# Optimization experiments

Hardware: AMD Instinct MI355X
Metric: run time of the kernel (lower is better)

## Reference

```python
import jax, jax.numpy as jnp
import numpy as np

CH = 64
INTER = 8  # max(64 // 8, 1)


def setup_inputs() -> dict:
    key = jax.random.key(0)
    ks = jax.random.split(key, 8)
    B, C, H, W = 4, CH, 64, 64
    x = jax.random.normal(ks[0], (B, C, H, W), dtype=jnp.float32)
    s = 1.0 / np.sqrt(C)
    Wq = jax.random.normal(ks[1], (INTER, C), dtype=jnp.float32) * s
    bq = jnp.zeros((INTER,), dtype=jnp.float32)
    Wk = jax.random.normal(ks[2], (INTER, C), dtype=jnp.float32) * s
    bk = jnp.zeros((INTER,), dtype=jnp.float32)
    Wv = jax.random.normal(ks[3], (C, C), dtype=jnp.float32) * s
    bv = jnp.zeros((C,), dtype=jnp.float32)
    gamma = jax.random.normal(ks[4], (1,), dtype=jnp.float32) * 0.1
    return {"x": x, "Wq": Wq, "bq": bq, "Wk": Wk, "bk": bk, "Wv": Wv, "bv": bv, "gamma": gamma}


def reference(x, Wq, bq, Wk, bk, Wv, bv, gamma):
    B, C, H, W = x.shape
    xf = x.reshape(B, C, H * W)  # [B, C, N]
    # 1x1 convs == per-pixel linear projections
    q = jnp.einsum('dc,bcn->bdn', Wq, xf) + bq[None, :, None]  # [B, d, N]
    k = jnp.einsum('dc,bcn->bdn', Wk, xf) + bk[None, :, None]  # [B, d, N]
    v = jnp.einsum('ec,bcn->ben', Wv, xf) + bv[None, :, None]  # [B, C, N]
    scale = 1.0 / np.sqrt(INTER).astype(np.float32)
    scores = jnp.einsum('bdi,bdj->bij', q, k) * scale  # [B, N, N]
    attn = jax.nn.softmax(scores, axis=-1)
    out = jnp.einsum('bcj,bij->bci', v, attn)  # value @ attn^T
    out = out.reshape(B, C, H, W)
    return gamma[0] * out + x
```

## Files before the change

### kernel.cpp

```cpp
#include <hip/hip_runtime.h>
#include <hip/hip_bf16.h>
#include <stdint.h>

#define BATCH 4
#define CCH   64
#define NPIX  4096
#define DQK   8
#define PXB   128

typedef __attribute__((ext_vector_type(8)))  short bf16x8;
typedef __attribute__((ext_vector_type(16))) float f32x16;
typedef __attribute__((ext_vector_type(4)))  uint32_t u32x4;

static __device__ __forceinline__ short f2bf(float f) {
    union { __hip_bfloat16 h; short s; } u;
    u.h = __float2bfloat16(f);
    return u.s;
}
static __device__ __forceinline__ uint32_t cvt_pk_bf16(float lo, float hi) {
    uint32_t r;
    asm("v_cvt_pk_bf16_f32 %0, %1, %2" : "=v"(r) : "v"(lo), "v"(hi));
    return r;
}

__global__ __launch_bounds__(256) void proj_kernel(
    const float* __restrict__ x,
    const float* __restrict__ Wq, const float* __restrict__ bq,
    const float* __restrict__ Wk, const float* __restrict__ bk,
    const float* __restrict__ Wv, const float* __restrict__ bv,
    short* __restrict__ qo, short* __restrict__ ko, short* __restrict__ vo)
{
    __shared__ float xs[CCH][PXB];
    __shared__ float wv_s[CCH][68];
    __shared__ float wq_s[CCH][DQK];
    __shared__ float wk_s[CCH][DQK];

    const int b  = blockIdx.x >> 5;
    const int n0 = (blockIdx.x & 31) * PXB;
    const int tid = threadIdx.x;

    for (int i = tid; i < CCH*CCH; i += 256) wv_s[i & 63][i >> 6] = Wv[i];
    for (int i = tid; i < CCH*DQK; i += 256) { wq_s[i & 63][i >> 6] = Wq[i]; wk_s[i & 63][i >> 6] = Wk[i]; }
    for (int i = tid; i < CCH*PXB; i += 256) {
        int c = i >> 7, p = i & 127;
        xs[c][p] = x[((size_t)b*CCH + c)*NPIX + n0 + p];
    }
    __syncthreads();

    const int p0 = tid & 31;
    const int g  = tid >> 5;
    const int e0 = g * 8;

    float av[4][8];
    float aq[4], ak[4];
    #pragma unroll
    for (int pi = 0; pi < 4; ++pi) {
        #pragma unroll
        for (int i = 0; i < 8; ++i) av[pi][i] = bv[e0 + i];
        aq[pi] = bq[g]; ak[pi] = bk[g];
    }

    for (int c = 0; c < CCH; ++c) {
        float4 w0 = *(const float4*)&wv_s[c][e0];
        float4 w1 = *(const float4*)&wv_s[c][e0 + 4];
        float wq = wq_s[c][g], wk = wk_s[c][g];
        #pragma unroll
        for (int pi = 0; pi < 4; ++pi) {
            float xv = xs[c][p0 + 32*pi];
            av[pi][0] += w0.x*xv; av[pi][1] += w0.y*xv;
            av[pi][2] += w0.z*xv; av[pi][3] += w0.w*xv;
            av[pi][4] += w1.x*xv; av[pi][5] += w1.y*xv;
            av[pi][6] += w1.z*xv; av[pi][7] += w1.w*xv;
            aq[pi] += wq*xv; ak[pi] += wk*xv;
        }
    }

    const float qscale = 0.51010407112635f;
    const size_t vb = (size_t)b * CCH * NPIX;
    #pragma unroll
    for (int pi = 0; pi < 4; ++pi) {
        const int px = n0 + p0 + 32*pi;
        #pragma unroll
        for (int i = 0; i < 8; ++i)
            vo[vb + (size_t)(e0 + i)*NPIX + px] = f2bf(av[pi][i]);
        const size_t qb = ((size_t)b*NPIX + px)*16 + g;
        qo[qb]     = f2bf(aq[pi] * qscale);
        qo[qb + 8] = 0;
        ko[qb]     = f2bf(ak[pi]);
        ko[qb + 8] = 0;
    }
}

__global__ __launch_bounds__(512, 2) void attn_kernel(
    const short* __restrict__ qg, const short* __restrict__ kg,
    const short* __restrict__ vg,
    const float* __restrict__ x, const float* __restrict__ gamma,
    float* __restrict__ outp)
{
    __shared__ float l_s[8][32];
    __shared__ float linv_s[32];
    __shared__ float acc_all[8][CCH][32];

    const int b  = blockIdx.x >> 7;
    const int i0 = (blockIdx.x & 127) << 5;
    const int tid  = threadIdx.x;
    const int wave = tid >> 6, lane = tid & 63;
    const int hi = lane >> 5, li = lane & 31;

    f32x16 z16;
    #pragma unroll
    for (int r = 0; r < 16; ++r) z16[r] = 0.f;

    const bf16x8 qf = *(const bf16x8*)&qg[((size_t)b*NPIX + i0 + li)*16 + hi*8];

    f32x16 acc0 = z16, acc1 = z16;
    float l_run = 0.f;

    const short* kp = kg + (size_t)b * NPIX * 16;
    const size_t vbase = (size_t)b * CCH * NPIX;
    const short* vrow0 = &vg[vbase + (size_t)li*NPIX];
    const short* vrow1 = vrow0 + (size_t)32*NPIX;

    const int jbeg = wave << 9;

    bf16x8 kc  = *(const bf16x8*)&kp[(size_t)(jbeg + li)*16 + hi*8];
    bf16x8 v00 = *(const bf16x8*)(vrow0 + jbeg + hi*8);
    bf16x8 v01 = *(const bf16x8*)(vrow0 + jbeg + 16 + hi*8);
    bf16x8 v10 = *(const bf16x8*)(vrow1 + jbeg + hi*8);
    bf16x8 v11 = *(const bf16x8*)(vrow1 + jbeg + 16 + hi*8);

    #pragma unroll 2
    for (int t = 0; t < 16; ++t) {
        const int j1 = jbeg + ((t + 1) & 15)*32;
        bf16x8 kn  = *(const bf16x8*)&kp[(size_t)(j1 + li)*16 + hi*8];
        bf16x8 n00 = *(const bf16x8*)(vrow0 + j1 + hi*8);
        bf16x8 n01 = *(const bf16x8*)(vrow0 + j1 + 16 + hi*8);
        bf16x8 n10 = *(const bf16x8*)(vrow1 + j1 + hi*8);
        bf16x8 n11 = *(const bf16x8*)(vrow1 + j1 + 16 + hi*8);

        f32x16 S = __builtin_amdgcn_mfma_f32_32x32x16_bf16(kc, qf, z16, 0, 0, 0);

        #pragma unroll
        for (int r = 0; r < 16; ++r) S[r] = __builtin_amdgcn_exp2f(S[r]);

        {
            float s0 = (S[0]+S[1]) + (S[2]+S[3]);
            float s1 = (S[4]+S[5]) + (S[6]+S[7]);
            float s2 = (S[8]+S[9]) + (S[10]+S[11]);
            float s3 = (S[12]+S[13]) + (S[14]+S[15]);
            l_run += (s0+s1) + (s2+s3);
        }

        uint32_t a01 = cvt_pk_bf16(S[0], S[1]);
        uint32_t a23 = cvt_pk_bf16(S[2], S[3]);
        uint32_t a45 = cvt_pk_bf16(S[4], S[5]);
        uint32_t a67 = cvt_pk_bf16(S[6], S[7]);
        uint32_t a89 = cvt_pk_bf16(S[8], S[9]);
        uint32_t aab = cvt_pk_bf16(S[10], S[11]);
        uint32_t acd = cvt_pk_bf16(S[12], S[13]);
        uint32_t aef = cvt_pk_bf16(S[14], S[15]);
        asm("v_permlane32_swap_b32 %0, %1" : "+v"(a01), "+v"(a45));
        asm("v_permlane32_swap_b32 %0, %1" : "+v"(a23), "+v"(a67));
        asm("v_permlane32_swap_b32 %0, %1" : "+v"(a89), "+v"(acd));
        asm("v_permlane32_swap_b32 %0, %1" : "+v"(aab), "+v"(aef));
        u32x4 pw0 = { a01, a23, a45, a67 };
        u32x4 pw1 = { a89, aab, acd, aef };
        bf16x8 b0 = __builtin_bit_cast(bf16x8, pw0);
        bf16x8 b1 = __builtin_bit_cast(bf16x8, pw1);

        __builtin_amdgcn_s_setprio(1);
        acc0 = __builtin_amdgcn_mfma_f32_32x32x16_bf16(v00, b0, acc0, 0, 0, 0);
        acc1 = __builtin_amdgcn_mfma_f32_32x32x16_bf16(v10, b0, acc1, 0, 0, 0);
        acc0 = __builtin_amdgcn_mfma_f32_32x32x16_bf16(v01, b1, acc0, 0, 0, 0);
        acc1 = __builtin_amdgcn_mfma_f32_32x32x16_bf16(v11, b1, acc1, 0, 0, 0);
        __builtin_amdgcn_s_setprio(0);

        kc = kn; v00 = n00; v01 = n01; v10 = n10; v11 = n11;
    }

    l_run += __shfl_xor(l_run, 32);
    if (hi == 0) l_s[wave][li] = l_run;
    #pragma unroll
    for (int r = 0; r < 16; ++r) {
        int row = (r & 3) + ((r >> 2) << 3) + (hi << 2);
        acc_all[wave][row][li]      = acc0[r];
        acc_all[wave][row + 32][li] = acc1[r];
    }
    __syncthreads();
    if (wave == 0 && hi == 0) {
        float L = 0.f;
        #pragma unroll
        for (int w = 0; w < 8; ++w) L += l_s[w][li];
        linv_s[li] = __builtin_amdgcn_rcpf(L);
    }
    __syncthreads();

    const float g0 = gamma[0];
    for (int idx = tid; idx < CCH*32; idx += 512) {
        int c = idx >> 5, i = idx & 31;
        float s = 0.f;
        #pragma unroll
        for (int w = 0; w < 8; ++w) s += acc_all[w][c][i];
        size_t gidx = vbase + (size_t)c*NPIX + i0 + i;
        outp[gidx] = g0 * (s * linv_s[i]) + x[gidx];
    }
}

extern "C" void kernel_launch(void* const* d_in, const int* in_sizes, int n_in,
                              void* d_out, int out_size, void* d_ws, size_t ws_size,
                              hipStream_t stream) {
    const float* x     = (const float*)d_in[0];
    const float* Wq    = (const float*)d_in[1];
    const float* bq    = (const float*)d_in[2];
    const float* Wk    = (const float*)d_in[3];
    const float* bk    = (const float*)d_in[4];
    const float* Wv    = (const float*)d_in[5];
    const float* bv    = (const float*)d_in[6];
    const float* gamma = (const float*)d_in[7];

    short* qo = (short*)d_ws;
    short* ko = qo + (size_t)BATCH*NPIX*16;
    short* vo = ko + (size_t)BATCH*NPIX*16;

    proj_kernel<<<BATCH*(NPIX/PXB), 256, 0, stream>>>(x, Wq, bq, Wk, bk, Wv, bv, qo, ko, vo);
    attn_kernel<<<BATCH*(NPIX/32), 512, 0, stream>>>(qo, ko, vo, x, gamma, (float*)d_out);
}
```

Baseline: 116.3 us.

## Split attention key range across blocks with separate merge kernel

Splits the key dimension of the attention into four chunks handled by separate 256-thread blocks, each writing partial unnormalized outputs and row sums to workspace. A new merge kernel sums the partials, normalizes, and applies the gamma residual. The software prefetch of K/V for the next iteration is also removed, so loads are issued inside the loop. This raises grid size and occupancy at the cost of an extra launch and about 16 MB of partial-buffer global traffic.

```diff
diff --git a/kernel.cpp b/kernel.cpp
--- a/kernel.cpp
+++ b/kernel.cpp
@@ -91,18 +91,18 @@
     }
 }
 
-__global__ __launch_bounds__(512, 2) void attn_kernel(
+__global__ __launch_bounds__(256, 4) void attn_main(
     const short* __restrict__ qg, const short* __restrict__ kg,
     const short* __restrict__ vg,
-    const float* __restrict__ x, const float* __restrict__ gamma,
-    float* __restrict__ outp)
+    float* __restrict__ part, float* __restrict__ lp)
 {
-    __shared__ float l_s[8][32];
-    __shared__ float linv_s[32];
-    __shared__ float acc_all[8][CCH][32];
-
-    const int b  = blockIdx.x >> 7;
-    const int i0 = (blockIdx.x & 127) << 5;
+    __shared__ float l_s[4][32];
+    __shared__ float acc_s[4][CCH][32];
+
+    const int jc = blockIdx.x & 3;
+    const int qt = (blockIdx.x >> 2) & 127;
+    const int b  = blockIdx.x >> 9;
+    const int i0 = qt << 5;
     const int tid  = threadIdx.x;
     const int wave = tid >> 6, lane = tid & 63;
     const int hi = lane >> 5, li = lane & 31;
@@ -121,24 +121,18 @@
     const short* vrow0 = &vg[vbase + (size_t)li*NPIX];
     const short* vrow1 = vrow0 + (size_t)32*NPIX;
 
-    const int jbeg = wave << 9;
-
-    bf16x8 kc  = *(const bf16x8*)&kp[(size_t)(jbeg + li)*16 + hi*8];
-    bf16x8 v00 = *(const bf16x8*)(vrow0 + jbeg + hi*8);
-    bf16x8 v01 = *(const bf16x8*)(vrow0 + jbeg + 16 + hi*8);
-    bf16x8 v10 = *(const bf16x8*)(vrow1 + jbeg + hi*8);
-    bf16x8 v11 = *(const bf16x8*)(vrow1 + jbeg + 16 + hi*8);
-
+    const int jbeg = (jc << 10) + (wave << 8);
     #pragma unroll 2
-    for (int t = 0; t < 16; ++t) {
-        const int j1 = jbeg + ((t + 1) & 15)*32;
-        bf16x8 kn  = *(const bf16x8*)&kp[(size_t)(j1 + li)*16 + hi*8];
-        bf16x8 n00 = *(const bf16x8*)(vrow0 + j1 + hi*8);
-        bf16x8 n01 = *(const bf16x8*)(vrow0 + j1 + 16 + hi*8);
-        bf16x8 n10 = *(const bf16x8*)(vrow1 + j1 + hi*8);
-        bf16x8 n11 = *(const bf16x8*)(vrow1 + j1 + 16 + hi*8);
-
-        f32x16 S = __builtin_amdgcn_mfma_f32_32x32x16_bf16(kc, qf, z16, 0, 0, 0);
+    for (int t = 0; t < 8; ++t) {
+        const int j0 = jbeg + t*32;
+
+        bf16x8 akf = *(const bf16x8*)&kp[(size_t)(j0 + li)*16 + hi*8];
+        f32x16 S = __builtin_amdgcn_mfma_f32_32x32x16_bf16(akf, qf, z16, 0, 0, 0);
+
+        bf16x8 av00 = *(const bf16x8*)(vrow0 + j0 + hi*8);
+        bf16x8 av01 = *(const bf16x8*)(vrow0 + j0 + 16 + hi*8);
+        bf16x8 av10 = *(const bf16x8*)(vrow1 + j0 + hi*8);
+        bf16x8 av11 = *(const bf16x8*)(vrow1 + j0 + 16 + hi*8);
 
         #pragma unroll
         for (int r = 0; r < 16; ++r) S[r] = __builtin_amdgcn_exp2f(S[r]);
@@ -169,13 +163,11 @@
         bf16x8 b1 = __builtin_bit_cast(bf16x8, pw1);
 
         __builtin_amdgcn_s_setprio(1);
-        acc0 = __builtin_amdgcn_mfma_f32_32x32x16_bf16(v00, b0, acc0, 0, 0, 0);
-        acc1 = __builtin_amdgcn_mfma_f32_32x32x16_bf16(v10, b0, acc1, 0, 0, 0);
-        acc0 = __builtin_amdgcn_mfma_f32_32x32x16_bf16(v01, b1, acc0, 0, 0, 0);
-        acc1 = __builtin_amdgcn_mfma_f32_32x32x16_bf16(v11, b1, acc1, 0, 0, 0);
+        acc0 = __builtin_amdgcn_mfma_f32_32x32x16_bf16(av00, b0, acc0, 0, 0, 0);
+        acc1 = __builtin_amdgcn_mfma_f32_32x32x16_bf16(av10, b0, acc1, 0, 0, 0);
+        acc0 = __builtin_amdgcn_mfma_f32_32x32x16_bf16(av01, b1, acc0, 0, 0, 0);
+        acc1 = __builtin_amdgcn_mfma_f32_32x32x16_bf16(av11, b1, acc1, 0, 0, 0);
         __builtin_amdgcn_s_setprio(0);
-
-        kc = kn; v00 = n00; v01 = n01; v10 = n10; v11 = n11;
     }
 
     l_run += __shfl_xor(l_run, 32);
@@ -183,24 +175,49 @@
     #pragma unroll
     for (int r = 0; r < 16; ++r) {
         int row = (r & 3) + ((r >> 2) << 3) + (hi << 2);
-        acc_all[wave][row][li]      = acc0[r];
-        acc_all[wave][row + 32][li] = acc1[r];
+        acc_s[wave][row][li]      = acc0[r];
+        acc_s[wave][row + 32][li] = acc1[r];
     }
     __syncthreads();
-    if (wave == 0 && hi == 0) {
-        float L = 0.f;
-        #pragma unroll
-        for (int w = 0; w < 8; ++w) L += l_s[w][li];
-        linv_s[li] = __builtin_amdgcn_rcpf(L);
+
+    float* pb = part + ((size_t)blockIdx.x) * (CCH*32);
+    for (int idx = tid; idx < CCH*32; idx += 256) {
+        int c = idx >> 5, i = idx & 31;
+        pb[idx] = acc_s[0][c][i] + acc_s[1][c][i] + acc_s[2][c][i] + acc_s[3][c][i];
+    }
+    if (tid < 32)
+        lp[((size_t)blockIdx.x)*32 + tid] =
+            l_s[0][tid] + l_s[1][tid] + l_s[2][tid] + l_s[3][tid];
+}
+
+__global__ __launch_bounds__(256) void merge_kernel(
+    const float* __restrict__ part, const float* __restrict__ lp,
+    const float* __restrict__ x, const float* __restrict__ gamma,
+    float* __restrict__ outp)
+{
+    __shared__ float linv_s[32];
+
+    const int qt = blockIdx.x & 127;
+    const int b  = blockIdx.x >> 7;
+    const int tid = threadIdx.x;
+
+    const size_t base = ((size_t)blockIdx.x) * 4 * (CCH*32);
+    const size_t lbase = ((size_t)blockIdx.x) * 4 * 32;
+
+    if (tid < 32) {
+        float L = lp[lbase + tid] + lp[lbase + 32 + tid]
+                + lp[lbase + 64 + tid] + lp[lbase + 96 + tid];
+        linv_s[tid] = __builtin_amdgcn_rcpf(L);
     }
     __syncthreads();
 
     const float g0 = gamma[0];
-    for (int idx = tid; idx < CCH*32; idx += 512) {
+    const size_t vbase = (size_t)b * CCH * NPIX;
+    const int i0 = qt << 5;
+    for (int idx = tid; idx < CCH*32; idx += 256) {
         int c = idx >> 5, i = idx & 31;
-        float s = 0.f;
-        #pragma unroll
-        for (int w = 0; w < 8; ++w) s += acc_all[w][c][i];
+        float s = part[base + idx] + part[base + 2048 + idx]
+                + part[base + 4096 + idx] + part[base + 6144 + idx];
         size_t gidx = vbase + (size_t)c*NPIX + i0 + i;
         outp[gidx] = g0 * (s * linv_s[i]) + x[gidx];
     }
@@ -221,7 +238,10 @@
     short* qo = (short*)d_ws;
     short* ko = qo + (size_t)BATCH*NPIX*16;
     short* vo = ko + (size_t)BATCH*NPIX*16;
+    float* part = (float*)(vo + (size_t)BATCH*CCH*NPIX);
+    float* lp   = part + (size_t)2048*CCH*32;
 
     proj_kernel<<<BATCH*(NPIX/PXB), 256, 0, stream>>>(x, Wq, bq, Wk, bk, Wv, bv, qo, ko, vo);
-    attn_kernel<<<BATCH*(NPIX/32), 512, 0, stream>>>(qo, ko, vo, x, gamma, (float*)d_out);
-}
+    attn_main<<<BATCH*(NPIX/32)*4, 256, 0, stream>>>(qo, ko, vo, part, lp);
+    merge_kernel<<<BATCH*(NPIX/32), 256, 0, stream>>>(part, lp, x, gamma, (float*)d_out);
+}
```

Result: slower. 124.4 us (+7.0%).

## Stage V tiles in swizzled LDS per window and shrink reduction buffer

Applied to the files above, without the earlier changes.

The attention kernel now loads each 256-column V window cooperatively into XOR-swizzled LDS, register-prefetching the next window, and has all waves read their V fragments from shared memory instead of each wave streaming its own disjoint 512-column slice from global memory. The cross-wave reduction reuses a 32KB buffer with a two-phase add, which cuts shared memory and allows a higher occupancy target in launch_bounds (512,4). The cost is two block-wide barriers per window and LDS traffic in the inner loop. The tighter register budget may also cause spills.

```diff
diff --git a/kernel.cpp b/kernel.cpp
--- a/kernel.cpp
+++ b/kernel.cpp
@@ -91,18 +91,22 @@
     }
 }
 
-__global__ __launch_bounds__(512, 2) void attn_kernel(
+__global__ __launch_bounds__(512, 4) void attn_kernel(
     const short* __restrict__ qg, const short* __restrict__ kg,
     const short* __restrict__ vg,
     const float* __restrict__ x, const float* __restrict__ gamma,
     float* __restrict__ outp)
 {
+    __shared__ __align__(16) char smem[32768];
     __shared__ float l_s[8][32];
     __shared__ float linv_s[32];
-    __shared__ float acc_all[8][CCH][32];
-
+
+    char*  vs_c = smem;
+    float* mbuf = (float*)smem;
+
+    const int qt = blockIdx.x & 127;
     const int b  = blockIdx.x >> 7;
-    const int i0 = (blockIdx.x & 127) << 5;
+    const int i0 = qt << 5;
     const int tid  = threadIdx.x;
     const int wave = tid >> 6, lane = tid & 63;
     const int hi = lane >> 5, li = lane & 31;
@@ -118,27 +122,48 @@
 
     const short* kp = kg + (size_t)b * NPIX * 16;
     const size_t vbase = (size_t)b * CCH * NPIX;
-    const short* vrow0 = &vg[vbase + (size_t)li*NPIX];
-    const short* vrow1 = vrow0 + (size_t)32*NPIX;
-
-    const int jbeg = wave << 9;
-
-    bf16x8 kc  = *(const bf16x8*)&kp[(size_t)(jbeg + li)*16 + hi*8];
-    bf16x8 v00 = *(const bf16x8*)(vrow0 + jbeg + hi*8);
-    bf16x8 v01 = *(const bf16x8*)(vrow0 + jbeg + 16 + hi*8);
-    bf16x8 v10 = *(const bf16x8*)(vrow1 + jbeg + hi*8);
-    bf16x8 v11 = *(const bf16x8*)(vrow1 + jbeg + 16 + hi*8);
-
-    #pragma unroll 2
-    for (int t = 0; t < 16; ++t) {
-        const int j1 = jbeg + ((t + 1) & 15)*32;
-        bf16x8 kn  = *(const bf16x8*)&kp[(size_t)(j1 + li)*16 + hi*8];
-        bf16x8 n00 = *(const bf16x8*)(vrow0 + j1 + hi*8);
-        bf16x8 n01 = *(const bf16x8*)(vrow0 + j1 + 16 + hi*8);
-        bf16x8 n10 = *(const bf16x8*)(vrow1 + j1 + hi*8);
-        bf16x8 n11 = *(const bf16x8*)(vrow1 + j1 + 16 + hi*8);
-
-        f32x16 S = __builtin_amdgcn_mfma_f32_32x32x16_bf16(kc, qf, z16, 0, 0, 0);
+
+    const int sc  = tid >> 3;
+    const short* vsrc = vg + vbase + (size_t)sc*NPIX + (tid & 7)*8;
+    const int   wb  = (tid & 7) * 16;
+    const int   swz = (sc & 15) << 4;
+    char* wp = vs_c + sc*512;
+
+    const int  rswz = (li & 15) << 4;
+    const int  rb0  = (wave << 6) + (hi << 4);
+    char* rp0 = vs_c + li*512;
+    char* rp1 = vs_c + (li + 32)*512;
+
+    int4 st0 = *(const int4*)(vsrc);
+    int4 st1 = *(const int4*)(vsrc + 64);
+    int4 st2 = *(const int4*)(vsrc + 128);
+    int4 st3 = *(const int4*)(vsrc + 192);
+    bf16x8 akf = *(const bf16x8*)&kp[(size_t)((wave << 5) + li)*16 + hi*8];
+
+    for (int win = 0; win < 16; ++win) {
+        *(int4*)(wp + ((wb +   0) ^ swz)) = st0;
+        *(int4*)(wp + ((wb + 128) ^ swz)) = st1;
+        *(int4*)(wp + ((wb + 256) ^ swz)) = st2;
+        *(int4*)(wp + ((wb + 384) ^ swz)) = st3;
+        if (win < 15) {
+            const short* ns = vsrc + (win + 1)*256;
+            st0 = *(const int4*)(ns);
+            st1 = *(const int4*)(ns + 64);
+            st2 = *(const int4*)(ns + 128);
+            st3 = *(const int4*)(ns + 192);
+        }
+        __syncthreads();
+
+        f32x16 S = __builtin_amdgcn_mfma_f32_32x32x16_bf16(akf, qf, z16, 0, 0, 0);
+        if (win < 15) {
+            const int jn = ((win + 1) << 8) + (wave << 5);
+            akf = *(const bf16x8*)&kp[(size_t)(jn + li)*16 + hi*8];
+        }
+
+        bf16x8 av00 = *(const bf16x8*)(rp0 + ((rb0     ) ^ rswz));
+        bf16x8 av01 = *(const bf16x8*)(rp0 + ((rb0 + 32) ^ rswz));
+        bf16x8 av10 = *(const bf16x8*)(rp1 + ((rb0     ) ^ rswz));
+        bf16x8 av11 = *(const bf16x8*)(rp1 + ((rb0 + 32) ^ rswz));
 
         #pragma unroll
         for (int r = 0; r < 16; ++r) S[r] = __builtin_amdgcn_exp2f(S[r]);
@@ -169,38 +194,46 @@
         bf16x8 b1 = __builtin_bit_cast(bf16x8, pw1);
 
         __builtin_amdgcn_s_setprio(1);
-        acc0 = __builtin_amdgcn_mfma_f32_32x32x16_bf16(v00, b0, acc0, 0, 0, 0);
-        acc1 = __builtin_amdgcn_mfma_f32_32x32x16_bf16(v10, b0, acc1, 0, 0, 0);
-        acc0 = __builtin_amdgcn_mfma_f32_32x32x16_bf16(v01, b1, acc0, 0, 0, 0);
-        acc1 = __builtin_amdgcn_mfma_f32_32x32x16_bf16(v11, b1, acc1, 0, 0, 0);
+        acc0 = __builtin_amdgcn_mfma_f32_32x32x16_bf16(av00, b0, acc0, 0, 0, 0);
+        acc1 = __builtin_amdgcn_mfma_f32_32x32x16_bf16(av10, b0, acc1, 0, 0, 0);
+        acc0 = __builtin_amdgcn_mfma_f32_32x32x16_bf16(av01, b1, acc0, 0, 0, 0);
+        acc1 = __builtin_amdgcn_mfma_f32_32x32x16_bf16(av11, b1, acc1, 0, 0, 0);
         __builtin_amdgcn_s_setprio(0);
-
-        kc = kn; v00 = n00; v01 = n01; v10 = n10; v11 = n11;
+        __syncthreads();
     }
 
     l_run += __shfl_xor(l_run, 32);
     if (hi == 0) l_s[wave][li] = l_run;
-    #pragma unroll
-    for (int r = 0; r < 16; ++r) {
-        int row = (r & 3) + ((r >> 2) << 3) + (hi << 2);
-        acc_all[wave][row][li]      = acc0[r];
-        acc_all[wave][row + 32][li] = acc1[r];
+
+    if (wave < 4) {
+        #pragma unroll
+        for (int r = 0; r < 16; ++r) {
+            int row = (r & 3) + ((r >> 2) << 3) + (hi << 2);
+            mbuf[(wave*64 + row)*32 + li]      = acc0[r];
+            mbuf[(wave*64 + row + 32)*32 + li] = acc1[r];
+        }
     }
     __syncthreads();
-    if (wave == 0 && hi == 0) {
+    if (wave >= 4) {
+        #pragma unroll
+        for (int r = 0; r < 16; ++r) {
+            int row = (r & 3) + ((r >> 2) << 3) + (hi << 2);
+            mbuf[((wave-4)*64 + row)*32 + li]      += acc0[r];
+            mbuf[((wave-4)*64 + row + 32)*32 + li] += acc1[r];
+        }
+    } else if (tid < 32) {
         float L = 0.f;
         #pragma unroll
-        for (int w = 0; w < 8; ++w) L += l_s[w][li];
-        linv_s[li] = __builtin_amdgcn_rcpf(L);
+        for (int w = 0; w < 8; ++w) L += l_s[w][tid];
+        linv_s[tid] = __builtin_amdgcn_rcpf(L);
     }
     __syncthreads();
 
     const float g0 = gamma[0];
     for (int idx = tid; idx < CCH*32; idx += 512) {
         int c = idx >> 5, i = idx & 31;
-        float s = 0.f;
-        #pragma unroll
-        for (int w = 0; w < 8; ++w) s += acc_all[w][c][i];
+        float s = mbuf[c*32 + i] + mbuf[(64 + c)*32 + i]
+                + mbuf[(128 + c)*32 + i] + mbuf[(192 + c)*32 + i];
         size_t gidx = vbase + (size_t)c*NPIX + i0 + i;
         outp[gidx] = g0 * (s * linv_s[i]) + x[gidx];
     }
```

After: 101.6 us. 12.6% less time.
